# Optimization experiments

Measured on AMD Instinct MI355X. Metric: run time of the kernel, lower is better.

The kernel has to match this reference:

```python
import jax, jax.numpy as jnp
import numpy as np

NUM_HEAD = 16
HEAD_DIM = 64
SEQ, BATCH, DMODEL = 2048, 2, 1024


def setup_inputs() -> dict:
    key = jax.random.key(0)
    ks = jax.random.split(key, 6)
    xavier = lambda k, shp: jax.random.uniform(
        k, shp, jnp.float32, -1.0, 1.0) * np.sqrt(6.0 / (shp[0] + shp[1]))
    query = jax.random.normal(ks[0], (SEQ, BATCH, DMODEL), jnp.float32)
    q_w = xavier(ks[1], (DMODEL, DMODEL))
    k_w = xavier(ks[2], (DMODEL, DMODEL))
    v_w = xavier(ks[3], (DMODEL, DMODEL))
    out_w = xavier(ks[4], (DMODEL, DMODEL))
    zeros = jnp.zeros((DMODEL,), jnp.float32)
    # causal mask: True = masked out (key position after query position)
    causal = jnp.triu(jnp.ones((SEQ, SEQ), bool), k=1)
    attn_mask = jnp.broadcast_to(causal, (BATCH, SEQ, SEQ))
    return {
        "query": query,
        "q_w": q_w, "q_b": zeros,
        "k_w": k_w, "k_b": zeros,
        "v_w": v_w, "v_b": zeros,
        "out_w": out_w, "out_b": zeros,
        "attn_mask": attn_mask,
    }


def reference(query, q_w, q_b, k_w, k_b, v_w, v_b, out_w, out_b, attn_mask):
    S, B, _ = query.shape
    H, Dh = NUM_HEAD, HEAD_DIM
    scale = 1.0 / np.sqrt(Dh)
    # self-attention: key = value = query
    q = (query @ q_w.T + q_b).reshape(S, B, H, Dh)
    k = (query @ k_w.T + k_b).reshape(S, B, H, Dh)
    v = (query @ v_w.T + v_b).reshape(S, B, H, Dh)
    # scores: [B, H, S(query), S(key)]
    scores = jnp.einsum('sbhd,tbhd->bhst', q, k) * scale
    scores = jnp.where(attn_mask[:, None, :, :], -jnp.inf, scores)
    attn = jax.nn.softmax(scores, axis=-1)
    # context: [S, B, H, Dh] -> [S, B, H*Dh]
    ctx = jnp.einsum('bhst,tbhd->sbhd', attn, v).reshape(S, B, H * Dh)
    return ctx @ out_w.T + out_b
```

## Files before the change

kernel.cpp:

```cpp
#include <hip/hip_runtime.h>
#include <hip/hip_bf16.h>

typedef __bf16 bf16;
typedef __attribute__((ext_vector_type(2))) __bf16 bf16x2;
typedef __attribute__((ext_vector_type(4))) __bf16 bf16x4;
typedef __attribute__((ext_vector_type(8))) __bf16 bf16x8;
typedef __attribute__((ext_vector_type(4))) float f32x4;

static_assert(sizeof(bf16x8) == 16, "bf16x8 must be 16B");

#define S_LEN 2048
#define BATCH_N 2
#define DM 1024
#define NHEAD 16
#define HDIM 64
#define LOG2E 1.44269504088896f

__device__ __forceinline__ void async_cp16(const void* g, void* l) {
    __builtin_amdgcn_global_load_lds(
        (const __attribute__((address_space(1))) void*)g,
        (__attribute__((address_space(3))) void*)l, 16, 0, 0);
}

__global__ __launch_bounds__(256)
void cvt_all(const float* __restrict__ q,
             const float* __restrict__ w0, const float* __restrict__ w1,
             const float* __restrict__ w2, const float* __restrict__ w3,
             bf16* __restrict__ Xb,
             bf16* __restrict__ W0, bf16* __restrict__ W1,
             bf16* __restrict__ W2, bf16* __restrict__ W3) {
    const int blk = blockIdx.x;
    const float* src;
    bf16* dst;
    size_t base;
    if (blk < 2048) {
        src = q; dst = Xb; base = (size_t)blk * 2048;
    } else {
        const int w = (blk - 2048) >> 9;
        const int r = (blk - 2048) & 511;
        base = (size_t)r * 2048;
        src = (w == 0) ? w0 : (w == 1) ? w1 : (w == 2) ? w2 : w3;
        dst = (w == 0) ? W0 : (w == 1) ? W1 : (w == 2) ? W2 : W3;
    }
    const size_t i = base + (size_t)threadIdx.x * 8;
    const f32x4 a = *(const f32x4*)(src + i);
    const f32x4 b = *(const f32x4*)(src + i + 4);
    bf16x8 r8;
    r8[0] = (bf16)a[0]; r8[1] = (bf16)a[1]; r8[2] = (bf16)a[2]; r8[3] = (bf16)a[3];
    r8[4] = (bf16)b[0]; r8[5] = (bf16)b[1]; r8[6] = (bf16)b[2]; r8[7] = (bf16)b[3];
    *(bf16x8*)(dst + i) = r8;
}

__device__ __forceinline__ void gemm_tile(const bf16* __restrict__ A,
                                          const bf16* __restrict__ W,
                                          int row0, int col0, int Kdim,
                                          f32x4 acc[4][4]) {
    __shared__ bf16 As[128 * 32];
    __shared__ bf16 Bs[128 * 32];
    const int tid  = threadIdx.x;
    const int lane = tid & 63;
    const int wv   = tid >> 6;
    const int wr = wv >> 1, wc = wv & 1;
    const int qr = lane & 15, quad = lane >> 4;

    const int srow = wv * 16 + (lane >> 2);
    const int scol = (lane & 3) * 8;
    const bf16* Ap = A + (size_t)(row0 + srow) * Kdim + scol;
    const bf16* Wp = W + (size_t)(col0 + srow) * Kdim + scol;
    bf16* lA0 = As + wv * 512;
    bf16* lA1 = As + 64 * 32 + wv * 512;
    bf16* lB0 = Bs + wv * 512;
    bf16* lB1 = Bs + 64 * 32 + wv * 512;

    const f32x4 fzero = {0.f, 0.f, 0.f, 0.f};
    #pragma unroll
    for (int mi = 0; mi < 4; ++mi)
        #pragma unroll
        for (int ni = 0; ni < 4; ++ni)
            acc[mi][ni] = fzero;

    for (int k0 = 0; k0 < Kdim; k0 += 32) {
        __syncthreads();
        async_cp16(Ap + k0, lA0);
        async_cp16(Ap + (size_t)64 * Kdim + k0, lA1);
        async_cp16(Wp + k0, lB0);
        async_cp16(Wp + (size_t)64 * Kdim + k0, lB1);
        __syncthreads();

        bf16x8 af[4], bfr[4];
        #pragma unroll
        for (int mi = 0; mi < 4; ++mi)
            af[mi] = *(const bf16x8*)(As + (wr * 64 + mi * 16 + qr) * 32 + quad * 8);
        #pragma unroll
        for (int ni = 0; ni < 4; ++ni)
            bfr[ni] = *(const bf16x8*)(Bs + (wc * 64 + ni * 16 + qr) * 32 + quad * 8);
        #pragma unroll
        for (int mi = 0; mi < 4; ++mi)
            #pragma unroll
            for (int ni = 0; ni < 4; ++ni)
                acc[mi][ni] = __builtin_amdgcn_mfma_f32_16x16x32_bf16(
                    af[mi], bfr[ni], acc[mi][ni], 0, 0, 0);
    }
}

__global__ __launch_bounds__(256)
void qkv_kernel(const bf16* __restrict__ X,
                const bf16* __restrict__ Wq, const float* __restrict__ bq,
                const bf16* __restrict__ Wk, const float* __restrict__ bk,
                const bf16* __restrict__ Wv, const float* __restrict__ bv,
                bf16* __restrict__ Q, bf16* __restrict__ Kt, bf16* __restrict__ Vt) {
    const int mat  = blockIdx.z;
    const bf16*  W    = (mat == 0) ? Wq : (mat == 1) ? Wk : Wv;
    const float* bias = (mat == 0) ? bq : (mat == 1) ? bk : bv;
    const int col0 = blockIdx.x * 128;
    const int row0 = blockIdx.y * 128;

    f32x4 acc[4][4];
    gemm_tile(X, W, row0, col0, DM, acc);

    const int lane = threadIdx.x & 63;
    const int wave = threadIdx.x >> 6;
    const int wr = wave >> 1, wc = wave & 1;
    const int qr = lane & 15, quad = lane >> 4;

    #pragma unroll
    for (int ni = 0; ni < 4; ++ni) {
        const int n  = col0 + wc * 64 + ni * 16 + qr;
        const float bn = bias[n];
        const int h = n >> 6, dh = n & 63;
        #pragma unroll
        for (int mi = 0; mi < 4; ++mi) {
            const int i0 = row0 + wr * 64 + mi * 16 + quad * 4;
            const float v0 = acc[mi][ni][0] + bn;
            const float v1 = acc[mi][ni][1] + bn;
            const float v2 = acc[mi][ni][2] + bn;
            const float v3 = acc[mi][ni][3] + bn;
            if (mat == 2) {
                const int s0 = i0 >> 1;
                bf16x2 e0 = {(bf16)v0, (bf16)v2};
                bf16x2 e1 = {(bf16)v1, (bf16)v3};
                *(bf16x2*)(Vt + ((size_t)h * HDIM + dh) * S_LEN + s0) = e0;
                *(bf16x2*)(Vt + ((size_t)(NHEAD + h) * HDIM + dh) * S_LEN + s0) = e1;
            } else {
                #pragma unroll
                for (int r = 0; r < 4; ++r) {
                    const int i = i0 + r;
                    const int s = i >> 1, b = i & 1;
                    const float v = (r == 0) ? v0 : (r == 1) ? v1 : (r == 2) ? v2 : v3;
                    if (mat == 0) {
                        Q[((size_t)(b * NHEAD + h) * S_LEN + s) * HDIM + dh] =
                            (bf16)(v * (0.125f * LOG2E));
                    } else {
                        Kt[((size_t)(b * NHEAD + h) * S_LEN + s) * HDIM + dh] = (bf16)v;
                    }
                }
            }
        }
    }
}

#define PLD 40
#define PT  640
#define RSTRIDE 36

#define MFMA(a, b, c) __builtin_amdgcn_mfma_f32_16x16x32_bf16(a, b, c, 0, 0, 0)
#define EX(x) __builtin_amdgcn_exp2f(x)

#define QK_TILE(j) \
    f32x4 sA##j = MFMA(k0, qlo##j, fzero); sA##j = MFMA(k1, qhi##j, sA##j); \
    f32x4 sB##j = MFMA(k2, qlo##j, fzero); sB##j = MFMA(k3, qhi##j, sB##j);

#define SFULL(j) do { \
    const float e0 = EX(sA##j[0]), e1 = EX(sA##j[1]), e2 = EX(sA##j[2]), e3 = EX(sA##j[3]); \
    const float f0 = EX(sB##j[0]), f1 = EX(sB##j[1]), f2 = EX(sB##j[2]), f3 = EX(sB##j[3]); \
    l##j += (e0 + e1 + e2 + e3) + (f0 + f1 + f2 + f3); \
    bf16x4 wa = {(bf16)e0, (bf16)e1, (bf16)e2, (bf16)e3}; \
    bf16x4 wb = {(bf16)f0, (bf16)f1, (bf16)f2, (bf16)f3}; \
    *(bf16x4*)(Pw + (j) * PT + qr * PLD + quad * 4)      = wa; \
    *(bf16x4*)(Pw + (j) * PT + qr * PLD + 16 + quad * 4) = wb; \
} while (0)

#define SMASK(j) do { \
    const int qrow = qb0 + 16 * (j) + qr; \
    const int ka = t * 32 + quad * 4; \
    const float e0 = (ka + 0  <= qrow) ? EX(sA##j[0]) : 0.f; \
    const float e1 = (ka + 1  <= qrow) ? EX(sA##j[1]) : 0.f; \
    const float e2 = (ka + 2  <= qrow) ? EX(sA##j[2]) : 0.f; \
    const float e3 = (ka + 3  <= qrow) ? EX(sA##j[3]) : 0.f; \
    const float f0 = (ka + 16 <= qrow) ? EX(sB##j[0]) : 0.f; \
    const float f1 = (ka + 17 <= qrow) ? EX(sB##j[1]) : 0.f; \
    const float f2 = (ka + 18 <= qrow) ? EX(sB##j[2]) : 0.f; \
    const float f3 = (ka + 19 <= qrow) ? EX(sB##j[3]) : 0.f; \
    l##j += (e0 + e1 + e2 + e3) + (f0 + f1 + f2 + f3); \
    bf16x4 wa = {(bf16)e0, (bf16)e1, (bf16)e2, (bf16)e3}; \
    bf16x4 wb = {(bf16)f0, (bf16)f1, (bf16)f2, (bf16)f3}; \
    *(bf16x4*)(Pw + (j) * PT + qr * PLD + quad * 4)      = wa; \
    *(bf16x4*)(Pw + (j) * PT + qr * PLD + 16 + quad * 4) = wb; \
} while (0)

__global__ __launch_bounds__(256)
void attn_part(const bf16* __restrict__ Q, const bf16* __restrict__ K,
               const bf16* __restrict__ Vt, bf16* __restrict__ ctx) {
    __shared__ __align__(16) char smem[27648 + 20480];
    const int lane = threadIdx.x & 63;
    const int wave = threadIdx.x >> 6;
    const int qr = lane & 15, quad = lane >> 4;
    const int bh = blockIdx.y;
    const int b = bh >> 4, h = bh & 15;

    const bf16* Qb = Q  + (size_t)bh * S_LEN * HDIM;
    const bf16* Kb = K  + (size_t)bh * S_LEN * HDIM;
    const bf16* Vb = Vt + (size_t)bh * HDIM * S_LEN;
    float* red = (float*)smem;
    bf16* Pw = (bf16*)(smem + 27648) + wave * (4 * PT);
    const f32x4 fzero = {0.f, 0.f, 0.f, 0.f};

    for (int phase = 0; phase < 2; ++phase) {
        const int qb = phase ? (31 - (int)blockIdx.x) : (int)blockIdx.x;
        const int qb0    = qb * 64;
        const int tdiag  = qb * 2;
        const int ntiles = 2 * qb + 2;

        const bf16x8 qlo0 = *(const bf16x8*)(Qb + (size_t)(qb0 + qr) * HDIM + quad * 8);
        const bf16x8 qhi0 = *(const bf16x8*)(Qb + (size_t)(qb0 + qr) * HDIM + quad * 8 + 32);
        const bf16x8 qlo1 = *(const bf16x8*)(Qb + (size_t)(qb0 + 16 + qr) * HDIM + quad * 8);
        const bf16x8 qhi1 = *(const bf16x8*)(Qb + (size_t)(qb0 + 16 + qr) * HDIM + quad * 8 + 32);
        const bf16x8 qlo2 = *(const bf16x8*)(Qb + (size_t)(qb0 + 32 + qr) * HDIM + quad * 8);
        const bf16x8 qhi2 = *(const bf16x8*)(Qb + (size_t)(qb0 + 32 + qr) * HDIM + quad * 8 + 32);
        const bf16x8 qlo3 = *(const bf16x8*)(Qb + (size_t)(qb0 + 48 + qr) * HDIM + quad * 8);
        const bf16x8 qhi3 = *(const bf16x8*)(Qb + (size_t)(qb0 + 48 + qr) * HDIM + quad * 8 + 32);

        f32x4 o0_0 = fzero, o0_1 = fzero, o0_2 = fzero, o0_3 = fzero;
        f32x4 o1_0 = fzero, o1_1 = fzero, o1_2 = fzero, o1_3 = fzero;
        f32x4 o2_0 = fzero, o2_1 = fzero, o2_2 = fzero, o2_3 = fzero;
        f32x4 o3_0 = fzero, o3_1 = fzero, o3_2 = fzero, o3_3 = fzero;
        float l0 = 0.f, l1 = 0.f, l2 = 0.f, l3 = 0.f;

        for (int t = wave; t < ntiles; t += 4) {
            const bf16* kp = Kb + ((size_t)t * 32 + qr) * HDIM + quad * 8;
            const bf16x8 k0 = *(const bf16x8*)(kp);
            const bf16x8 k1 = *(const bf16x8*)(kp + 32);
            const bf16x8 k2 = *(const bf16x8*)(kp + 16 * HDIM);
            const bf16x8 k3 = *(const bf16x8*)(kp + 16 * HDIM + 32);
            const bf16* vp = Vb + (size_t)qr * S_LEN + t * 32 + quad * 8;
            const bf16x8 v0 = *(const bf16x8*)(vp);
            const bf16x8 v1 = *(const bf16x8*)(vp + 16 * S_LEN);
            const bf16x8 v2 = *(const bf16x8*)(vp + 32 * S_LEN);
            const bf16x8 v3 = *(const bf16x8*)(vp + 48 * S_LEN);

            if (t < tdiag) {
                QK_TILE(0); SFULL(0);
                QK_TILE(1); SFULL(1);
                QK_TILE(2); SFULL(2);
                QK_TILE(3); SFULL(3);
            } else {
                QK_TILE(0); SMASK(0);
                QK_TILE(1); SMASK(1);
                QK_TILE(2); SMASK(2);
                QK_TILE(3); SMASK(3);
            }

            const bf16x8 pf0 = *(const bf16x8*)(Pw + 0 * PT + qr * PLD + quad * 8);
            const bf16x8 pf1 = *(const bf16x8*)(Pw + 1 * PT + qr * PLD + quad * 8);
            const bf16x8 pf2 = *(const bf16x8*)(Pw + 2 * PT + qr * PLD + quad * 8);
            const bf16x8 pf3 = *(const bf16x8*)(Pw + 3 * PT + qr * PLD + quad * 8);
            o0_0 = MFMA(v0, pf0, o0_0); o0_1 = MFMA(v1, pf0, o0_1);
            o0_2 = MFMA(v2, pf0, o0_2); o0_3 = MFMA(v3, pf0, o0_3);
            o1_0 = MFMA(v0, pf1, o1_0); o1_1 = MFMA(v1, pf1, o1_1);
            o1_2 = MFMA(v2, pf1, o1_2); o1_3 = MFMA(v3, pf1, o1_3);
            o2_0 = MFMA(v0, pf2, o2_0); o2_1 = MFMA(v1, pf2, o2_1);
            o2_2 = MFMA(v2, pf2, o2_2); o2_3 = MFMA(v3, pf2, o2_3);
            o3_0 = MFMA(v0, pf3, o3_0); o3_1 = MFMA(v1, pf3, o3_1);
            o3_2 = MFMA(v2, pf3, o3_2); o3_3 = MFMA(v3, pf3, o3_3);
        }

        __syncthreads();
        if (wave != 0) {
            float* rp = red + ((size_t)(wave - 1) * 64 + lane) * RSTRIDE;
            *(f32x4*)(rp +  0) = o0_0; *(f32x4*)(rp +  4) = o0_1;
            *(f32x4*)(rp +  8) = o0_2; *(f32x4*)(rp + 12) = o0_3;
            *(f32x4*)(rp + 16) = o1_0; *(f32x4*)(rp + 20) = o1_1;
            *(f32x4*)(rp + 24) = o1_2; *(f32x4*)(rp + 28) = o1_3;
            rp[32] = l0; rp[33] = l1;
        }
        __syncthreads();
        if (wave == 0) {
            #pragma unroll
            for (int w = 0; w < 3; ++w) {
                const float* rp = red + ((size_t)w * 64 + lane) * RSTRIDE;
                o0_0 += *(const f32x4*)(rp +  0); o0_1 += *(const f32x4*)(rp +  4);
                o0_2 += *(const f32x4*)(rp +  8); o0_3 += *(const f32x4*)(rp + 12);
                o1_0 += *(const f32x4*)(rp + 16); o1_1 += *(const f32x4*)(rp + 20);
                o1_2 += *(const f32x4*)(rp + 24); o1_3 += *(const f32x4*)(rp + 28);
                l0 += rp[32]; l1 += rp[33];
            }
        }
        __syncthreads();
        if (wave != 0) {
            float* rp = red + ((size_t)(wave - 1) * 64 + lane) * RSTRIDE;
            *(f32x4*)(rp +  0) = o2_0; *(f32x4*)(rp +  4) = o2_1;
            *(f32x4*)(rp +  8) = o2_2; *(f32x4*)(rp + 12) = o2_3;
            *(f32x4*)(rp + 16) = o3_0; *(f32x4*)(rp + 20) = o3_1;
            *(f32x4*)(rp + 24) = o3_2; *(f32x4*)(rp + 28) = o3_3;
            rp[32] = l2; rp[33] = l3;
        }
        __syncthreads();
        if (wave == 0) {
            #pragma unroll
            for (int w = 0; w < 3; ++w) {
                const float* rp = red + ((size_t)w * 64 + lane) * RSTRIDE;
                o2_0 += *(const f32x4*)(rp +  0); o2_1 += *(const f32x4*)(rp +  4);
                o2_2 += *(const f32x4*)(rp +  8); o2_3 += *(const f32x4*)(rp + 12);
                o3_0 += *(const f32x4*)(rp + 16); o3_1 += *(const f32x4*)(rp + 20);
                o3_2 += *(const f32x4*)(rp + 24); o3_3 += *(const f32x4*)(rp + 28);
                l2 += rp[32]; l3 += rp[33];
            }
            l0 += __shfl_xor(l0, 16); l0 += __shfl_xor(l0, 32);
            l1 += __shfl_xor(l1, 16); l1 += __shfl_xor(l1, 32);
            l2 += __shfl_xor(l2, 16); l2 += __shfl_xor(l2, 32);
            l3 += __shfl_xor(l3, 16); l3 += __shfl_xor(l3, 32);
            const float n0 = 1.f / l0, n1 = 1.f / l1, n2 = 1.f / l2, n3 = 1.f / l3;

            #define CWRITE(ov, ni_, jrow_, nf_) do { \
                bf16x4 cc = {(bf16)(ov[0] * (nf_)), (bf16)(ov[1] * (nf_)), \
                             (bf16)(ov[2] * (nf_)), (bf16)(ov[3] * (nf_))}; \
                const int s_ = qb0 + (jrow_) * 16 + qr; \
                *(bf16x4*)(ctx + ((size_t)s_ * BATCH_N + b) * DM \
                           + h * HDIM + (ni_) * 16 + quad * 4) = cc; \
            } while (0)
            CWRITE(o0_0, 0, 0, n0); CWRITE(o0_1, 1, 0, n0);
            CWRITE(o0_2, 2, 0, n0); CWRITE(o0_3, 3, 0, n0);
            CWRITE(o1_0, 0, 1, n1); CWRITE(o1_1, 1, 1, n1);
            CWRITE(o1_2, 2, 1, n1); CWRITE(o1_3, 3, 1, n1);
            CWRITE(o2_0, 0, 2, n2); CWRITE(o2_1, 1, 2, n2);
            CWRITE(o2_2, 2, 2, n2); CWRITE(o2_3, 3, 2, n2);
            CWRITE(o3_0, 0, 3, n3); CWRITE(o3_1, 1, 3, n3);
            CWRITE(o3_2, 2, 3, n3); CWRITE(o3_3, 3, 3, n3);
            #undef CWRITE
        }
    }
}

__global__ __launch_bounds__(256)
void proj_kernel(const bf16* __restrict__ X, const bf16* __restrict__ W,
                 const float* __restrict__ bias, float* __restrict__ out) {
    const int col0 = blockIdx.x * 128;
    const int row0 = blockIdx.y * 128;
    f32x4 acc[4][4];
    gemm_tile(X, W, row0, col0, DM, acc);

    const int lane = threadIdx.x & 63;
    const int wave = threadIdx.x >> 6;
    const int wr = wave >> 1, wc = wave & 1;
    const int qr = lane & 15, quad = lane >> 4;

    #pragma unroll
    for (int ni = 0; ni < 4; ++ni) {
        const int n = col0 + wc * 64 + ni * 16 + qr;
        const float bn = bias[n];
        #pragma unroll
        for (int mi = 0; mi < 4; ++mi) {
            #pragma unroll
            for (int r = 0; r < 4; ++r) {
                const int i = row0 + wr * 64 + mi * 16 + quad * 4 + r;
                out[(size_t)i * DM + n] = acc[mi][ni][r] + bn;
            }
        }
    }
}

extern "C" void kernel_launch(void* const* d_in, const int* in_sizes, int n_in,
                              void* d_out, int out_size, void* d_ws, size_t ws_size,
                              hipStream_t stream) {
    (void)in_sizes; (void)n_in; (void)out_size; (void)ws_size;
    const float* query = (const float*)d_in[0];
    const float* q_w   = (const float*)d_in[1];
    const float* q_b   = (const float*)d_in[2];
    const float* k_w   = (const float*)d_in[3];
    const float* k_b   = (const float*)d_in[4];
    const float* v_w   = (const float*)d_in[5];
    const float* v_b   = (const float*)d_in[6];
    const float* out_w = (const float*)d_in[7];
    const float* out_b = (const float*)d_in[8];

    char* ws = (char*)d_ws;
    bf16*  Qb   = (bf16*)(ws);
    bf16*  Kb   = (bf16*)(ws + ((size_t)8  << 20));
    bf16*  Vt   = (bf16*)(ws + ((size_t)16 << 20));
    bf16*  ctx  = (bf16*)(ws + ((size_t)24 << 20));
    bf16*  Wob  = (bf16*)(ws + ((size_t)32 << 20));
    bf16*  Xb   = (bf16*)(ws + ((size_t)34 << 20));
    bf16*  Wqb  = (bf16*)(ws + ((size_t)42 << 20));
    bf16*  Wkb  = (bf16*)(ws + ((size_t)44 << 20));
    bf16*  Wvb  = (bf16*)(ws + ((size_t)46 << 20));
    float* out  = (float*)d_out;

    dim3 blk(256);
    cvt_all<<<dim3(2048 + 4 * 512), blk, 0, stream>>>(
        query, q_w, k_w, v_w, out_w, Xb, Wqb, Wkb, Wvb, Wob);

    qkv_kernel<<<dim3(DM / 128, (S_LEN * BATCH_N) / 128, 3), blk, 0, stream>>>(
        Xb, Wqb, q_b, Wkb, k_b, Wvb, v_b, Qb, Kb, Vt);
    attn_part<<<dim3(16, BATCH_N * NHEAD), blk, 0, stream>>>(Qb, Kb, Vt, ctx);
    proj_kernel<<<dim3(DM / 128, (S_LEN * BATCH_N) / 128), blk, 0, stream>>>(
        ctx, Wob, out_b, out);
}
```

Baseline: 219.1 us.

## Prefetch next K/V tile in registers, raise MFMA priority, remap grid to 1D

The attention kernel now loads the K and V fragments for the next tile into registers while the current tile's QK, softmax and PV MFMAs run, so global load latency overlaps with compute. The MFMA block is wrapped in s_setprio to favour matrix issue. The grid becomes 1D with head index in the low bits, so consecutive blocks cover different heads, which changes how blocks spread across XCDs and caches. The cost is higher register pressure from the extra eight bf16x8 prefetch registers, which may reduce occupancy.

```diff
diff --git a/kernel.cpp b/kernel.cpp
--- a/kernel.cpp
+++ b/kernel.cpp
@@ -205,7 +205,8 @@
     const int lane = threadIdx.x & 63;
     const int wave = threadIdx.x >> 6;
     const int qr = lane & 15, quad = lane >> 4;
-    const int bh = blockIdx.y;
+    const int bh = blockIdx.x & 31;
+    const int bx = blockIdx.x >> 5;
     const int b = bh >> 4, h = bh & 15;
 
     const bf16* Qb = Q  + (size_t)bh * S_LEN * HDIM;
@@ -216,7 +217,7 @@
     const f32x4 fzero = {0.f, 0.f, 0.f, 0.f};
 
     for (int phase = 0; phase < 2; ++phase) {
-        const int qb = phase ? (31 - (int)blockIdx.x) : (int)blockIdx.x;
+        const int qb = phase ? (31 - bx) : bx;
         const int qb0    = qb * 64;
         const int tdiag  = qb * 2;
         const int ntiles = 2 * qb + 2;
@@ -236,17 +237,32 @@
         f32x4 o3_0 = fzero, o3_1 = fzero, o3_2 = fzero, o3_3 = fzero;
         float l0 = 0.f, l1 = 0.f, l2 = 0.f, l3 = 0.f;
 
-        for (int t = wave; t < ntiles; t += 4) {
+        int t = wave;
+        bf16x8 k0, k1, k2, k3, v0, v1, v2, v3;
+        if (t < ntiles) {
             const bf16* kp = Kb + ((size_t)t * 32 + qr) * HDIM + quad * 8;
-            const bf16x8 k0 = *(const bf16x8*)(kp);
-            const bf16x8 k1 = *(const bf16x8*)(kp + 32);
-            const bf16x8 k2 = *(const bf16x8*)(kp + 16 * HDIM);
-            const bf16x8 k3 = *(const bf16x8*)(kp + 16 * HDIM + 32);
+            k0 = *(const bf16x8*)(kp);
+            k1 = *(const bf16x8*)(kp + 32);
+            k2 = *(const bf16x8*)(kp + 16 * HDIM);
+            k3 = *(const bf16x8*)(kp + 16 * HDIM + 32);
             const bf16* vp = Vb + (size_t)qr * S_LEN + t * 32 + quad * 8;
-            const bf16x8 v0 = *(const bf16x8*)(vp);
-            const bf16x8 v1 = *(const bf16x8*)(vp + 16 * S_LEN);
-            const bf16x8 v2 = *(const bf16x8*)(vp + 32 * S_LEN);
-            const bf16x8 v3 = *(const bf16x8*)(vp + 48 * S_LEN);
+            v0 = *(const bf16x8*)(vp);
+            v1 = *(const bf16x8*)(vp + 16 * S_LEN);
+            v2 = *(const bf16x8*)(vp + 32 * S_LEN);
+            v3 = *(const bf16x8*)(vp + 48 * S_LEN);
+        }
+        for (; t < ntiles; t += 4) {
+            const int tn = (t + 4 < ntiles) ? (t + 4) : t;
+            const bf16* kpn = Kb + ((size_t)tn * 32 + qr) * HDIM + quad * 8;
+            const bf16x8 nk0 = *(const bf16x8*)(kpn);
+            const bf16x8 nk1 = *(const bf16x8*)(kpn + 32);
+            const bf16x8 nk2 = *(const bf16x8*)(kpn + 16 * HDIM);
+            const bf16x8 nk3 = *(const bf16x8*)(kpn + 16 * HDIM + 32);
+            const bf16* vpn = Vb + (size_t)qr * S_LEN + tn * 32 + quad * 8;
+            const bf16x8 nv0 = *(const bf16x8*)(vpn);
+            const bf16x8 nv1 = *(const bf16x8*)(vpn + 16 * S_LEN);
+            const bf16x8 nv2 = *(const bf16x8*)(vpn + 32 * S_LEN);
+            const bf16x8 nv3 = *(const bf16x8*)(vpn + 48 * S_LEN);
 
             if (t < tdiag) {
                 QK_TILE(0); SFULL(0);
@@ -264,6 +280,7 @@
             const bf16x8 pf1 = *(const bf16x8*)(Pw + 1 * PT + qr * PLD + quad * 8);
             const bf16x8 pf2 = *(const bf16x8*)(Pw + 2 * PT + qr * PLD + quad * 8);
             const bf16x8 pf3 = *(const bf16x8*)(Pw + 3 * PT + qr * PLD + quad * 8);
+            __builtin_amdgcn_s_setprio(1);
             o0_0 = MFMA(v0, pf0, o0_0); o0_1 = MFMA(v1, pf0, o0_1);
             o0_2 = MFMA(v2, pf0, o0_2); o0_3 = MFMA(v3, pf0, o0_3);
             o1_0 = MFMA(v0, pf1, o1_0); o1_1 = MFMA(v1, pf1, o1_1);
@@ -272,6 +289,10 @@
             o2_2 = MFMA(v2, pf2, o2_2); o2_3 = MFMA(v3, pf2, o2_3);
             o3_0 = MFMA(v0, pf3, o3_0); o3_1 = MFMA(v1, pf3, o3_1);
             o3_2 = MFMA(v2, pf3, o3_2); o3_3 = MFMA(v3, pf3, o3_3);
+            __builtin_amdgcn_s_setprio(0);
+
+            k0 = nk0; k1 = nk1; k2 = nk2; k3 = nk3;
+            v0 = nv0; v1 = nv1; v2 = nv2; v3 = nv3;
         }
 
         __syncthreads();
@@ -401,7 +422,7 @@
 
     qkv_kernel<<<dim3(DM / 128, (S_LEN * BATCH_N) / 128, 3), blk, 0, stream>>>(
         Xb, Wqb, q_b, Wkb, k_b, Wvb, v_b, Qb, Kb, Vt);
-    attn_part<<<dim3(16, BATCH_N * NHEAD), blk, 0, stream>>>(Qb, Kb, Vt, ctx);
+    attn_part<<<dim3(512), blk, 0, stream>>>(Qb, Kb, Vt, ctx);
     proj_kernel<<<dim3(DM / 128, (S_LEN * BATCH_N) / 128), blk, 0, stream>>>(
         ctx, Wob, out_b, out);
 }
```

Result: no change. 215.6 us (-1.6%).

## Split attention by query rows per wave with double-buffered async K/V staging

Applied to the files above, without the earlier changes.

The attention kernel now gives each wave its own 16 query rows instead of splitting key tiles across waves. That removes the cross-wave LDS reduction and the paired-phase scheme, and the grid grows to 1024 blocks ordered longest-first. K and V tiles are copied into XOR-swizzled, double-buffered LDS with async global-to-LDS loads shared by all four waves, and s_setprio is raised around the PV MFMAs. In exchange there is a __syncthreads on every tile, and each block now handles only one query block.

```diff
diff --git a/kernel.cpp b/kernel.cpp
--- a/kernel.cpp
+++ b/kernel.cpp
@@ -161,184 +161,127 @@
 
 #define PLD 40
 #define PT  640
-#define RSTRIDE 36
 
 #define MFMA(a, b, c) __builtin_amdgcn_mfma_f32_16x16x32_bf16(a, b, c, 0, 0, 0)
 #define EX(x) __builtin_amdgcn_exp2f(x)
-
-#define QK_TILE(j) \
-    f32x4 sA##j = MFMA(k0, qlo##j, fzero); sA##j = MFMA(k1, qhi##j, sA##j); \
-    f32x4 sB##j = MFMA(k2, qlo##j, fzero); sB##j = MFMA(k3, qhi##j, sB##j);
-
-#define SFULL(j) do { \
-    const float e0 = EX(sA##j[0]), e1 = EX(sA##j[1]), e2 = EX(sA##j[2]), e3 = EX(sA##j[3]); \
-    const float f0 = EX(sB##j[0]), f1 = EX(sB##j[1]), f2 = EX(sB##j[2]), f3 = EX(sB##j[3]); \
-    l##j += (e0 + e1 + e2 + e3) + (f0 + f1 + f2 + f3); \
-    bf16x4 wa = {(bf16)e0, (bf16)e1, (bf16)e2, (bf16)e3}; \
-    bf16x4 wb = {(bf16)f0, (bf16)f1, (bf16)f2, (bf16)f3}; \
-    *(bf16x4*)(Pw + (j) * PT + qr * PLD + quad * 4)      = wa; \
-    *(bf16x4*)(Pw + (j) * PT + qr * PLD + 16 + quad * 4) = wb; \
-} while (0)
-
-#define SMASK(j) do { \
-    const int qrow = qb0 + 16 * (j) + qr; \
-    const int ka = t * 32 + quad * 4; \
-    const float e0 = (ka + 0  <= qrow) ? EX(sA##j[0]) : 0.f; \
-    const float e1 = (ka + 1  <= qrow) ? EX(sA##j[1]) : 0.f; \
-    const float e2 = (ka + 2  <= qrow) ? EX(sA##j[2]) : 0.f; \
-    const float e3 = (ka + 3  <= qrow) ? EX(sA##j[3]) : 0.f; \
-    const float f0 = (ka + 16 <= qrow) ? EX(sB##j[0]) : 0.f; \
-    const float f1 = (ka + 17 <= qrow) ? EX(sB##j[1]) : 0.f; \
-    const float f2 = (ka + 18 <= qrow) ? EX(sB##j[2]) : 0.f; \
-    const float f3 = (ka + 19 <= qrow) ? EX(sB##j[3]) : 0.f; \
-    l##j += (e0 + e1 + e2 + e3) + (f0 + f1 + f2 + f3); \
-    bf16x4 wa = {(bf16)e0, (bf16)e1, (bf16)e2, (bf16)e3}; \
-    bf16x4 wb = {(bf16)f0, (bf16)f1, (bf16)f2, (bf16)f3}; \
-    *(bf16x4*)(Pw + (j) * PT + qr * PLD + quad * 4)      = wa; \
-    *(bf16x4*)(Pw + (j) * PT + qr * PLD + 16 + quad * 4) = wb; \
-} while (0)
 
 __global__ __launch_bounds__(256)
 void attn_part(const bf16* __restrict__ Q, const bf16* __restrict__ K,
                const bf16* __restrict__ Vt, bf16* __restrict__ ctx) {
-    __shared__ __align__(16) char smem[27648 + 20480];
-    const int lane = threadIdx.x & 63;
-    const int wave = threadIdx.x >> 6;
+    __shared__ __align__(16) char smem[21504];
+    const int tid  = threadIdx.x;
+    const int lane = tid & 63;
+    const int wave = tid >> 6;
     const int qr = lane & 15, quad = lane >> 4;
-    const int bh = blockIdx.y;
+    const int bh = blockIdx.x & 31;
+    const int bx = blockIdx.x >> 5;
     const int b = bh >> 4, h = bh & 15;
 
-    const bf16* Qb = Q  + (size_t)bh * S_LEN * HDIM;
-    const bf16* Kb = K  + (size_t)bh * S_LEN * HDIM;
-    const bf16* Vb = Vt + (size_t)bh * HDIM * S_LEN;
-    float* red = (float*)smem;
-    bf16* Pw = (bf16*)(smem + 27648) + wave * (4 * PT);
+    const char* Kg = (const char*)(K  + (size_t)bh * S_LEN * HDIM);
+    const char* Vg = (const char*)(Vt + (size_t)bh * HDIM * S_LEN);
+    const bf16* Qb = Q + (size_t)bh * S_LEN * HDIM;
+    char* Ksm = smem;
+    char* Vsm = smem + 8192;
+    bf16* Pw  = (bf16*)(smem + 16384) + wave * PT;
     const f32x4 fzero = {0.f, 0.f, 0.f, 0.f};
 
-    for (int phase = 0; phase < 2; ++phase) {
-        const int qb = phase ? (31 - (int)blockIdx.x) : (int)blockIdx.x;
-        const int qb0    = qb * 64;
-        const int tdiag  = qb * 2;
-        const int ntiles = 2 * qb + 2;
-
-        const bf16x8 qlo0 = *(const bf16x8*)(Qb + (size_t)(qb0 + qr) * HDIM + quad * 8);
-        const bf16x8 qhi0 = *(const bf16x8*)(Qb + (size_t)(qb0 + qr) * HDIM + quad * 8 + 32);
-        const bf16x8 qlo1 = *(const bf16x8*)(Qb + (size_t)(qb0 + 16 + qr) * HDIM + quad * 8);
-        const bf16x8 qhi1 = *(const bf16x8*)(Qb + (size_t)(qb0 + 16 + qr) * HDIM + quad * 8 + 32);
-        const bf16x8 qlo2 = *(const bf16x8*)(Qb + (size_t)(qb0 + 32 + qr) * HDIM + quad * 8);
-        const bf16x8 qhi2 = *(const bf16x8*)(Qb + (size_t)(qb0 + 32 + qr) * HDIM + quad * 8 + 32);
-        const bf16x8 qlo3 = *(const bf16x8*)(Qb + (size_t)(qb0 + 48 + qr) * HDIM + quad * 8);
-        const bf16x8 qhi3 = *(const bf16x8*)(Qb + (size_t)(qb0 + 48 + qr) * HDIM + quad * 8 + 32);
-
-        f32x4 o0_0 = fzero, o0_1 = fzero, o0_2 = fzero, o0_3 = fzero;
-        f32x4 o1_0 = fzero, o1_1 = fzero, o1_2 = fzero, o1_3 = fzero;
-        f32x4 o2_0 = fzero, o2_1 = fzero, o2_2 = fzero, o2_3 = fzero;
-        f32x4 o3_0 = fzero, o3_1 = fzero, o3_2 = fzero, o3_3 = fzero;
-        float l0 = 0.f, l1 = 0.f, l2 = 0.f, l3 = 0.f;
-
-        for (int t = wave; t < ntiles; t += 4) {
-            const bf16* kp = Kb + ((size_t)t * 32 + qr) * HDIM + quad * 8;
-            const bf16x8 k0 = *(const bf16x8*)(kp);
-            const bf16x8 k1 = *(const bf16x8*)(kp + 32);
-            const bf16x8 k2 = *(const bf16x8*)(kp + 16 * HDIM);
-            const bf16x8 k3 = *(const bf16x8*)(kp + 16 * HDIM + 32);
-            const bf16* vp = Vb + (size_t)qr * S_LEN + t * 32 + quad * 8;
-            const bf16x8 v0 = *(const bf16x8*)(vp);
-            const bf16x8 v1 = *(const bf16x8*)(vp + 16 * S_LEN);
-            const bf16x8 v2 = *(const bf16x8*)(vp + 32 * S_LEN);
-            const bf16x8 v3 = *(const bf16x8*)(vp + 48 * S_LEN);
-
-            if (t < tdiag) {
-                QK_TILE(0); SFULL(0);
-                QK_TILE(1); SFULL(1);
-                QK_TILE(2); SFULL(2);
-                QK_TILE(3); SFULL(3);
-            } else {
-                QK_TILE(0); SMASK(0);
-                QK_TILE(1); SMASK(1);
-                QK_TILE(2); SMASK(2);
-                QK_TILE(3); SMASK(3);
-            }
-
-            const bf16x8 pf0 = *(const bf16x8*)(Pw + 0 * PT + qr * PLD + quad * 8);
-            const bf16x8 pf1 = *(const bf16x8*)(Pw + 1 * PT + qr * PLD + quad * 8);
-            const bf16x8 pf2 = *(const bf16x8*)(Pw + 2 * PT + qr * PLD + quad * 8);
-            const bf16x8 pf3 = *(const bf16x8*)(Pw + 3 * PT + qr * PLD + quad * 8);
-            o0_0 = MFMA(v0, pf0, o0_0); o0_1 = MFMA(v1, pf0, o0_1);
-            o0_2 = MFMA(v2, pf0, o0_2); o0_3 = MFMA(v3, pf0, o0_3);
-            o1_0 = MFMA(v0, pf1, o1_0); o1_1 = MFMA(v1, pf1, o1_1);
-            o1_2 = MFMA(v2, pf1, o1_2); o1_3 = MFMA(v3, pf1, o1_3);
-            o2_0 = MFMA(v0, pf2, o2_0); o2_1 = MFMA(v1, pf2, o2_1);
-            o2_2 = MFMA(v2, pf2, o2_2); o2_3 = MFMA(v3, pf2, o2_3);
-            o3_0 = MFMA(v0, pf3, o3_0); o3_1 = MFMA(v1, pf3, o3_1);
-            o3_2 = MFMA(v2, pf3, o3_2); o3_3 = MFMA(v3, pf3, o3_3);
+    const int qb     = 31 - bx;
+    const int qb0    = qb * 64;
+    const int tdiag  = qb * 2;
+    const int ntiles = 2 * qb + 2;
+
+    const int d16   = tid * 16;
+    const int ksrow = d16 >> 7;
+    const int ksoff = (d16 & 127) ^ ((ksrow & 7) << 4);
+    const int vsrow = d16 >> 6;
+    const int vsoff = (d16 & 63) ^ ((vsrow & 3) << 4);
+    const size_t kgbase = (size_t)ksrow * 128 + ksoff;
+    const size_t vgbase = (size_t)vsrow * (S_LEN * 2) + vsoff;
+
+#define STAGE(t_, bi_) do { \
+    async_cp16(Kg + (size_t)(t_) * 4096 + kgbase, Ksm + (bi_) * 4096 + wave * 1024); \
+    async_cp16(Vg + (size_t)(t_) * 64   + vgbase, Vsm + (bi_) * 4096 + wave * 1024); \
+} while (0)
+
+    const int qrow0 = qb0 + wave * 16;
+    const bf16x8 qlo = *(const bf16x8*)(Qb + (size_t)(qrow0 + qr) * HDIM + quad * 8);
+    const bf16x8 qhi = *(const bf16x8*)(Qb + (size_t)(qrow0 + qr) * HDIM + quad * 8 + 32);
+
+    f32x4 o0 = fzero, o1 = fzero, o2 = fzero, o3 = fzero;
+    float l = 0.f;
+
+    STAGE(0, 0);
+    __syncthreads();
+
+    const int sK = (qr & 7) << 4;
+    const int sV = (qr & 3) << 4;
+
+    for (int t = 0; t < ntiles; ++t) {
+        const int cur = t & 1;
+        if (t + 1 < ntiles) STAGE(t + 1, cur ^ 1);
+
+        const char* Kc = Ksm + cur * 4096;
+        const char* Vc = Vsm + cur * 4096;
+        const bf16x8 k0 = *(const bf16x8*)(Kc + qr * 128        + ((quad * 16)      ^ sK));
+        const bf16x8 k1 = *(const bf16x8*)(Kc + qr * 128        + ((quad * 16 + 64) ^ sK));
+        const bf16x8 k2 = *(const bf16x8*)(Kc + (16 + qr) * 128 + ((quad * 16)      ^ sK));
+        const bf16x8 k3 = *(const bf16x8*)(Kc + (16 + qr) * 128 + ((quad * 16 + 64) ^ sK));
+        const bf16x8 v0 = *(const bf16x8*)(Vc + qr * 64         + ((quad * 16) ^ sV));
+        const bf16x8 v1 = *(const bf16x8*)(Vc + (16 + qr) * 64  + ((quad * 16) ^ sV));
+        const bf16x8 v2 = *(const bf16x8*)(Vc + (32 + qr) * 64  + ((quad * 16) ^ sV));
+        const bf16x8 v3 = *(const bf16x8*)(Vc + (48 + qr) * 64  + ((quad * 16) ^ sV));
+
+        f32x4 sA = MFMA(k0, qlo, fzero); sA = MFMA(k1, qhi, sA);
+        f32x4 sB = MFMA(k2, qlo, fzero); sB = MFMA(k3, qhi, sB);
+
+        if (t < tdiag) {
+            const float e0 = EX(sA[0]), e1 = EX(sA[1]), e2 = EX(sA[2]), e3 = EX(sA[3]);
+            const float f0 = EX(sB[0]), f1 = EX(sB[1]), f2 = EX(sB[2]), f3 = EX(sB[3]);
+            l += (e0 + e1 + e2 + e3) + (f0 + f1 + f2 + f3);
+            bf16x4 wa = {(bf16)e0, (bf16)e1, (bf16)e2, (bf16)e3};
+            bf16x4 wb = {(bf16)f0, (bf16)f1, (bf16)f2, (bf16)f3};
+            *(bf16x4*)(Pw + qr * PLD + quad * 4)      = wa;
+            *(bf16x4*)(Pw + qr * PLD + 16 + quad * 4) = wb;
+        } else {
+            const int qrow = qrow0 + qr;
+            const int ka = t * 32 + quad * 4;
+            const float e0 = (ka + 0  <= qrow) ? EX(sA[0]) : 0.f;
+            const float e1 = (ka + 1  <= qrow) ? EX(sA[1]) : 0.f;
+            const float e2 = (ka + 2  <= qrow) ? EX(sA[2]) : 0.f;
+            const float e3 = (ka + 3  <= qrow) ? EX(sA[3]) : 0.f;
+            const float f0 = (ka + 16 <= qrow) ? EX(sB[0]) : 0.f;
+            const float f1 = (ka + 17 <= qrow) ? EX(sB[1]) : 0.f;
+            const float f2 = (ka + 18 <= qrow) ? EX(sB[2]) : 0.f;
+            const float f3 = (ka + 19 <= qrow) ? EX(sB[3]) : 0.f;
+            l += (e0 + e1 + e2 + e3) + (f0 + f1 + f2 + f3);
+            bf16x4 wa = {(bf16)e0, (bf16)e1, (bf16)e2, (bf16)e3};
+            bf16x4 wb = {(bf16)f0, (bf16)f1, (bf16)f2, (bf16)f3};
+            *(bf16x4*)(Pw + qr * PLD + quad * 4)      = wa;
+            *(bf16x4*)(Pw + qr * PLD + 16 + quad * 4) = wb;
         }
 
+        const bf16x8 pf = *(const bf16x8*)(Pw + qr * PLD + quad * 8);
+        __builtin_amdgcn_s_setprio(1);
+        o0 = MFMA(v0, pf, o0); o1 = MFMA(v1, pf, o1);
+        o2 = MFMA(v2, pf, o2); o3 = MFMA(v3, pf, o3);
+        __builtin_amdgcn_s_setprio(0);
+
         __syncthreads();
-        if (wave != 0) {
-            float* rp = red + ((size_t)(wave - 1) * 64 + lane) * RSTRIDE;
-            *(f32x4*)(rp +  0) = o0_0; *(f32x4*)(rp +  4) = o0_1;
-            *(f32x4*)(rp +  8) = o0_2; *(f32x4*)(rp + 12) = o0_3;
-            *(f32x4*)(rp + 16) = o1_0; *(f32x4*)(rp + 20) = o1_1;
-            *(f32x4*)(rp + 24) = o1_2; *(f32x4*)(rp + 28) = o1_3;
-            rp[32] = l0; rp[33] = l1;
-        }
-        __syncthreads();
-        if (wave == 0) {
-            #pragma unroll
-            for (int w = 0; w < 3; ++w) {
-                const float* rp = red + ((size_t)w * 64 + lane) * RSTRIDE;
-                o0_0 += *(const f32x4*)(rp +  0); o0_1 += *(const f32x4*)(rp +  4);
-                o0_2 += *(const f32x4*)(rp +  8); o0_3 += *(const f32x4*)(rp + 12);
-                o1_0 += *(const f32x4*)(rp + 16); o1_1 += *(const f32x4*)(rp + 20);
-                o1_2 += *(const f32x4*)(rp + 24); o1_3 += *(const f32x4*)(rp + 28);
-                l0 += rp[32]; l1 += rp[33];
-            }
-        }
-        __syncthreads();
-        if (wave != 0) {
-            float* rp = red + ((size_t)(wave - 1) * 64 + lane) * RSTRIDE;
-            *(f32x4*)(rp +  0) = o2_0; *(f32x4*)(rp +  4) = o2_1;
-            *(f32x4*)(rp +  8) = o2_2; *(f32x4*)(rp + 12) = o2_3;
-            *(f32x4*)(rp + 16) = o3_0; *(f32x4*)(rp + 20) = o3_1;
-            *(f32x4*)(rp + 24) = o3_2; *(f32x4*)(rp + 28) = o3_3;
-            rp[32] = l2; rp[33] = l3;
-        }
-        __syncthreads();
-        if (wave == 0) {
-            #pragma unroll
-            for (int w = 0; w < 3; ++w) {
-                const float* rp = red + ((size_t)w * 64 + lane) * RSTRIDE;
-                o2_0 += *(const f32x4*)(rp +  0); o2_1 += *(const f32x4*)(rp +  4);
-                o2_2 += *(const f32x4*)(rp +  8); o2_3 += *(const f32x4*)(rp + 12);
-                o3_0 += *(const f32x4*)(rp + 16); o3_1 += *(const f32x4*)(rp + 20);
-                o3_2 += *(const f32x4*)(rp + 24); o3_3 += *(const f32x4*)(rp + 28);
-                l2 += rp[32]; l3 += rp[33];
-            }
-            l0 += __shfl_xor(l0, 16); l0 += __shfl_xor(l0, 32);
-            l1 += __shfl_xor(l1, 16); l1 += __shfl_xor(l1, 32);
-            l2 += __shfl_xor(l2, 16); l2 += __shfl_xor(l2, 32);
-            l3 += __shfl_xor(l3, 16); l3 += __shfl_xor(l3, 32);
-            const float n0 = 1.f / l0, n1 = 1.f / l1, n2 = 1.f / l2, n3 = 1.f / l3;
-
-            #define CWRITE(ov, ni_, jrow_, nf_) do { \
-                bf16x4 cc = {(bf16)(ov[0] * (nf_)), (bf16)(ov[1] * (nf_)), \
-                             (bf16)(ov[2] * (nf_)), (bf16)(ov[3] * (nf_))}; \
-                const int s_ = qb0 + (jrow_) * 16 + qr; \
-                *(bf16x4*)(ctx + ((size_t)s_ * BATCH_N + b) * DM \
-                           + h * HDIM + (ni_) * 16 + quad * 4) = cc; \
-            } while (0)
-            CWRITE(o0_0, 0, 0, n0); CWRITE(o0_1, 1, 0, n0);
-            CWRITE(o0_2, 2, 0, n0); CWRITE(o0_3, 3, 0, n0);
-            CWRITE(o1_0, 0, 1, n1); CWRITE(o1_1, 1, 1, n1);
-            CWRITE(o1_2, 2, 1, n1); CWRITE(o1_3, 3, 1, n1);
-            CWRITE(o2_0, 0, 2, n2); CWRITE(o2_1, 1, 2, n2);
-            CWRITE(o2_2, 2, 2, n2); CWRITE(o2_3, 3, 2, n2);
-            CWRITE(o3_0, 0, 3, n3); CWRITE(o3_1, 1, 3, n3);
-            CWRITE(o3_2, 2, 3, n3); CWRITE(o3_3, 3, 3, n3);
-            #undef CWRITE
-        }
-    }
+    }
+#undef STAGE
+
+    l += __shfl_xor(l, 16); l += __shfl_xor(l, 32);
+    const float n = 1.f / l;
+
+    const int s_ = qrow0 + qr;
+    bf16* cp = ctx + ((size_t)s_ * BATCH_N + b) * DM + h * HDIM + quad * 4;
+    #define CW(ov, vi_) do { \
+        bf16x4 cc = {(bf16)(ov[0] * n), (bf16)(ov[1] * n), \
+                     (bf16)(ov[2] * n), (bf16)(ov[3] * n)}; \
+        *(bf16x4*)(cp + (vi_) * 16) = cc; \
+    } while (0)
+    CW(o0, 0); CW(o1, 1); CW(o2, 2); CW(o3, 3);
+    #undef CW
 }
 
 __global__ __launch_bounds__(256)
@@ -401,7 +344,7 @@
 
     qkv_kernel<<<dim3(DM / 128, (S_LEN * BATCH_N) / 128, 3), blk, 0, stream>>>(
         Xb, Wqb, q_b, Wkb, k_b, Wvb, v_b, Qb, Kb, Vt);
-    attn_part<<<dim3(16, BATCH_N * NHEAD), blk, 0, stream>>>(Qb, Kb, Vt, ctx);
+    attn_part<<<dim3(1024), blk, 0, stream>>>(Qb, Kb, Vt, ctx);
     proj_kernel<<<dim3(DM / 128, (S_LEN * BATCH_N) / 128), blk, 0, stream>>>(
         ctx, Wob, out_b, out);
 }
```

Result: faster. 207.3 us (-5.4%).
